# Kernel tuning notes

Hardware: AMD Instinct MI355X
Metric: run time of the kernel (lower is better)

Reference implementation:

```python
import jax, jax.numpy as jnp
import numpy as np

DIM = 1024
HEADS = 16
HEAD_DIM = DIM // HEADS


def rotate_half(x):
    x1, x2 = jnp.split(x, 2, axis=-1)
    return jnp.concatenate((-x2, x1), axis=-1)


def rope_tables(T, D, dtype=jnp.float32):
    inv_freq = 1.0 / (10000.0 ** (jnp.arange(0, D, 2, dtype=jnp.float32) / D))
    t = jnp.arange(T, dtype=jnp.float32)
    freqs = jnp.einsum('i,j->ij', t, inv_freq)  # [T, D/2]
    emb = jnp.concatenate((freqs, freqs), axis=-1)  # [T, D]
    return emb.astype(dtype), jnp.cos(emb).astype(dtype), jnp.sin(emb).astype(dtype)


def setup_inputs() -> dict:
    key = jax.random.key(0)
    kx, kq, kk, kv, ko = jax.random.split(key, 5)
    B, T = 2, 4096
    scale = 1.0 / np.sqrt(DIM)
    x = jax.random.normal(kx, (B, T, DIM), dtype=jnp.float32)
    wq = jax.random.normal(kq, (DIM, DIM), dtype=jnp.float32) * scale
    wk = jax.random.normal(kk, (DIM, DIM), dtype=jnp.float32) * scale
    wv = jax.random.normal(kv, (DIM, DIM), dtype=jnp.float32) * scale
    wo = jax.random.normal(ko, (DIM, DIM), dtype=jnp.float32) * scale
    return {"x": x, "wq": wq, "wk": wk, "wv": wv, "wo": wo}


def reference(x, wq, wk, wv, wo):
    B, T, C = x.shape
    H, D = HEADS, HEAD_DIM
    # projections; nn.Linear applies x @ W^T
    q = (x @ wq.T).reshape(B, T, H, D).transpose(0, 2, 1, 3)  # [B,H,T,D]
    k = (x @ wk.T).reshape(B, T, H, D).transpose(0, 2, 1, 3)
    v = (x @ wv.T).reshape(B, T, H, D).transpose(0, 2, 1, 3)
    _, cos, sin = rope_tables(T, D, x.dtype)
    cos = cos[None, None]  # [1,1,T,D]
    sin = sin[None, None]
    q = q * cos + rotate_half(q) * sin
    k = k * cos + rotate_half(k) * sin
    scores = jnp.einsum('bhtd,bhsd->bhts', q, k) / jnp.sqrt(jnp.asarray(D, x.dtype))
    attn = jax.nn.softmax(scores, axis=-1)
    out = jnp.einsum('bhts,bhsd->bhtd', attn, v)
    out = out.transpose(0, 2, 1, 3).reshape(B, T, C)
    return out @ wo.T
```

## Files before the change

kernel.cpp:

```cpp
#include <hip/hip_runtime.h>
#include <hip/hip_bf16.h>
#include <math.h>


typedef __attribute__((ext_vector_type(8))) short short8;
typedef __attribute__((ext_vector_type(4))) short short4v;
typedef __attribute__((ext_vector_type(4))) float floatx4;

using bf16 = __hip_bfloat16;

static constexpr int T_ = 4096;
static constexpr int C_ = 1024;
static constexpr int M_ = 8192;
static constexpr float QSCALE = 0.125f * 1.44269504088896340736f;

#if __has_builtin(__builtin_amdgcn_mfma_f32_16x16x16bf16_1k)
#define USE_K16 1
#else
#define USE_K16 0
#endif

#if __has_builtin(__builtin_amdgcn_exp2f)
#define EXP2 __builtin_amdgcn_exp2f
#else
#define EXP2 exp2f
#endif

__device__ __forceinline__ floatx4 mfma16(short8 a, short8 b, floatx4 c) {
    return __builtin_amdgcn_mfma_f32_16x16x32_bf16(a, b, c, 0, 0, 0);
}
#if USE_K16
__device__ __forceinline__ floatx4 mfma_k16(short4v a, short4v b, floatx4 c) {
    return __builtin_amdgcn_mfma_f32_16x16x16bf16_1k(a, b, c, 0, 0, 0);
}
#endif

__device__ __forceinline__ short8 ld8(const bf16* p) {
    return *reinterpret_cast<const short8*>(p);
}
__device__ __forceinline__ short4v ld4(const bf16* p) {
    return *reinterpret_cast<const short4v*>(p);
}
__device__ __forceinline__ void st8(bf16* p, short8 v) {
    *reinterpret_cast<short8*>(p) = v;
}
__device__ __forceinline__ unsigned short f2bf(float x) {
    bf16 h = __float2bfloat16(x);
    return reinterpret_cast<unsigned short&>(h);
}

__device__ __forceinline__ int pack2bf(float a, float b, unsigned sel) {
    const unsigned ua = __float_as_uint(a) + 0x8000u;
    const unsigned ub = __float_as_uint(b) + 0x8000u;
    int r;
    asm("v_perm_b32 %0, %1, %2, %3" : "=v"(r) : "v"(ub), "v"(ua), "s"(sel));
    return r;
}
__device__ __forceinline__ short4v i2s4(int lo, int hi) {
    union { int2 i; short4v s; } u;
    u.i.x = lo; u.i.y = hi;
    return u.s;
}
__device__ __forceinline__ short8 i2s8(int a, int b, int c, int d) {
    union { int4 i; short8 s; } u;
    u.i.x = a; u.i.y = b; u.i.z = c; u.i.w = d;
    return u.s;
}

__device__ __forceinline__ void cp16(const bf16* g, bf16* l) {
    __builtin_amdgcn_global_load_lds(
        (const __attribute__((address_space(1))) void*)g,
        (__attribute__((address_space(3))) void*)l, 16, 0, 0);
}

__global__ __launch_bounds__(256)
void prep_kernel(const float* __restrict__ x,
                 const float* __restrict__ wq, const float* __restrict__ wk,
                 const float* __restrict__ wv, const float* __restrict__ wo,
                 bf16* __restrict__ xb, bf16* __restrict__ wqb,
                 float2* __restrict__ CS) {
    const int blk = blockIdx.x;
    if (blk < 6144) {
        const float* in;
        bf16* out;
        int i;
        if (blk < 4096) {
            i = blk * 256 + threadIdx.x;
            in = x; out = xb;
        } else {
            i = (blk - 4096) * 256 + threadIdx.x;
            const int seg = i >> 17;
            const int off = i & 131071;
            in = (seg == 0) ? wq : (seg == 1) ? wk : (seg == 2) ? wv : wo;
            out = wqb + (size_t)i * 8 - (size_t)off * 8;
            i = off;
        }
        const float4* p = reinterpret_cast<const float4*>(in) + (size_t)i * 2;
        const float4 a = p[0];
        const float4 b = p[1];
        short8 v;
        v[0] = (short)f2bf(a.x); v[1] = (short)f2bf(a.y);
        v[2] = (short)f2bf(a.z); v[3] = (short)f2bf(a.w);
        v[4] = (short)f2bf(b.x); v[5] = (short)f2bf(b.y);
        v[6] = (short)f2bf(b.z); v[7] = (short)f2bf(b.w);
        *(reinterpret_cast<short8*>(out) + i) = v;
    } else {
        const int i = (blk - 6144) * 256 + threadIdx.x;
        const int t = i >> 5;
        const int j = i & 31;
        const float inv_freq = expf(-(float)j * 0.28782313662425575f);
        float s, c;
        sincosf((float)t * inv_freq, &s, &c);
        CS[i] = make_float2(c, s);
    }
}

__global__ __launch_bounds__(256)
void gemm128_kernel(const bf16* __restrict__ A, const bf16* __restrict__ W,
                    void* __restrict__ out, int mode, int ntile, int cpx) {
    const int orig = blockIdx.x;
    const int swz  = (orig & 7) * cpx + (orig >> 3);
    const int m0   = (swz / ntile) * 128;
    const int n0   = (swz % ntile) * 128;
    const int tid  = threadIdx.x;
    const int lane = tid & 63;
    const int wave = tid >> 6;
    const int quad = lane >> 4;
    const int lr   = lane & 15;
    const int wr   = (wave >> 1) * 64;
    const int wc   = (wave & 1) * 64;

    __shared__ __align__(16) bf16 Als[2][128 * 32];
    __shared__ __align__(16) bf16 Bls[2][128 * 32];

    const int srow = tid >> 2;
    const int scol = (tid & 3) * 8;

    floatx4 acc[4][4];
#pragma unroll
    for (int i = 0; i < 4; ++i)
#pragma unroll
        for (int j = 0; j < 4; ++j) acc[i][j] = floatx4{0.f, 0.f, 0.f, 0.f};

    const bf16* Ab = A + (size_t)m0 * C_;
    const bf16* Wb = W + (size_t)n0 * C_;

#pragma unroll
    for (int j = 0; j < 2; ++j) {
        const int row = srow + j * 64;
        cp16(Ab + (size_t)row * C_ + scol, &Als[0][(j * 256 + tid) * 8]);
        cp16(Wb + (size_t)row * C_ + scol, &Bls[0][(j * 256 + tid) * 8]);
    }
    __syncthreads();

    for (int k = 0; k < C_; k += 32) {
        const int buf = (k >> 5) & 1;
        if (k + 32 < C_) {
            const int nb = buf ^ 1;
#pragma unroll
            for (int j = 0; j < 2; ++j) {
                const int row = srow + j * 64;
                cp16(Ab + (size_t)row * C_ + k + 32 + scol,
                     &Als[nb][(j * 256 + tid) * 8]);
                cp16(Wb + (size_t)row * C_ + k + 32 + scol,
                     &Bls[nb][(j * 256 + tid) * 8]);
            }
        }

        short8 a[4], b[4];
#pragma unroll
        for (int i = 0; i < 4; ++i)
            a[i] = ld8(&Als[buf][(wr + i * 16 + lr) * 32 + quad * 8]);
#pragma unroll
        for (int j = 0; j < 4; ++j)
            b[j] = ld8(&Bls[buf][(wc + j * 16 + lr) * 32 + quad * 8]);
#pragma unroll
        for (int i = 0; i < 4; ++i)
#pragma unroll
            for (int j = 0; j < 4; ++j) acc[i][j] = mfma16(a[i], b[j], acc[i][j]);

        __syncthreads();
    }

    if (mode == 0) {
        bf16* ob = (bf16*)out;
#pragma unroll
        for (int j = 0; j < 4; ++j) {
            const int col = n0 + wc + j * 16 + lr;
#pragma unroll
            for (int i = 0; i < 4; ++i)
#pragma unroll
                for (int r = 0; r < 4; ++r) {
                    const int m = m0 + wr + i * 16 + quad * 4 + r;
                    ob[(size_t)m * C_ + col] = __float2bfloat16(acc[i][j][r]);
                }
        }
    } else {
        float* of = (float*)out;
#pragma unroll
        for (int j = 0; j < 4; ++j) {
            const int col = n0 + wc + j * 16 + lr;
#pragma unroll
            for (int i = 0; i < 4; ++i)
#pragma unroll
                for (int r = 0; r < 4; ++r) {
                    const int m = m0 + wr + i * 16 + quad * 4 + r;
                    of[(size_t)m * C_ + col] = acc[i][j][r];
                }
        }
    }
}

__global__ __launch_bounds__(256)
void gemm_qkv_kernel(const bf16* __restrict__ A, const bf16* __restrict__ W,
                     bf16* __restrict__ Qbase, const float2* __restrict__ CS) {
    const int orig = blockIdx.x;
    const int swz  = (orig & 7) * 192 + (orig >> 3);
    const int m0   = (swz / 24) * 128;
    const int n0g  = (swz % 24) * 128;
    const int tid  = threadIdx.x;
    const int lane = tid & 63;
    const int wave = tid >> 6;
    const int quad = lane >> 4;
    const int lr   = lane & 15;
    const int wr   = (wave >> 1) * 64;
    const int wc   = (wave & 1) * 64;

    __shared__ __align__(16) bf16 Als[2][128 * 32];
    __shared__ __align__(16) bf16 Bls[2][128 * 32];

    const int srow = tid >> 2;
    const int scol = (tid & 3) * 8;

    floatx4 acc[4][4];
#pragma unroll
    for (int i = 0; i < 4; ++i)
#pragma unroll
        for (int j = 0; j < 4; ++j) acc[i][j] = floatx4{0.f, 0.f, 0.f, 0.f};

    const bf16* Ab = A + (size_t)m0 * C_;
    const bf16* Wb = W + (size_t)n0g * C_;

#pragma unroll
    for (int j = 0; j < 2; ++j) {
        const int row = srow + j * 64;
        cp16(Ab + (size_t)row * C_ + scol, &Als[0][(j * 256 + tid) * 8]);
        cp16(Wb + (size_t)row * C_ + scol, &Bls[0][(j * 256 + tid) * 8]);
    }
    __syncthreads();

    for (int k = 0; k < C_; k += 32) {
        const int buf = (k >> 5) & 1;
        if (k + 32 < C_) {
            const int nb = buf ^ 1;
#pragma unroll
            for (int j = 0; j < 2; ++j) {
                const int row = srow + j * 64;
                cp16(Ab + (size_t)row * C_ + k + 32 + scol,
                     &Als[nb][(j * 256 + tid) * 8]);
                cp16(Wb + (size_t)row * C_ + k + 32 + scol,
                     &Bls[nb][(j * 256 + tid) * 8]);
            }
        }

        short8 a[4], b[4];
#pragma unroll
        for (int i = 0; i < 4; ++i)
            a[i] = ld8(&Als[buf][(wr + i * 16 + lr) * 32 + quad * 8]);
#pragma unroll
        for (int j = 0; j < 4; ++j)
            b[j] = ld8(&Bls[buf][(wc + j * 16 + lr) * 32 + quad * 8]);
#pragma unroll
        for (int i = 0; i < 4; ++i)
#pragma unroll
            for (int j = 0; j < 4; ++j) acc[i][j] = mfma16(a[i], b[j], acc[i][j]);

        __syncthreads();
    }

    const int seg = n0g >> 10;
    const int n0  = n0g & 1023;
    if (seg < 2) {
        bf16* ob = Qbase + (size_t)seg * M_ * C_;
        const float scale = (seg == 0) ? QSCALE : 1.0f;
        const int tb = (m0 & 4095) + wr + quad * 4;
#pragma unroll
        for (int j = 0; j < 2; ++j) {
            const int col  = n0 + wc + j * 16 + lr;
            const int jcol = j * 16 + lr;
#pragma unroll
            for (int i = 0; i < 4; ++i) {
#pragma unroll
                for (int r = 0; r < 4; ++r) {
                    const int t = tb + i * 16 + r;
                    const float2 cs = CS[t * 32 + jcol];
                    const float q1 = acc[i][j][r];
                    const float q2 = acc[i][j + 2][r];
                    const int m = m0 + wr + i * 16 + quad * 4 + r;
                    ob[(size_t)m * C_ + col] =
                        __float2bfloat16((q1 * cs.x - q2 * cs.y) * scale);
                    ob[(size_t)m * C_ + col + 32] =
                        __float2bfloat16((q2 * cs.x + q1 * cs.y) * scale);
                }
            }
        }
    } else {
        unsigned short* ob = (unsigned short*)(Qbase + (size_t)2 * M_ * C_);
        const int b2 = m0 >> 12;
#pragma unroll
        for (int j = 0; j < 4; ++j) {
            const int n = n0 + wc + j * 16 + lr;
            const int h = n >> 6;
            const int d = n & 63;
#pragma unroll
            for (int i = 0; i < 4; ++i) {
                const int t0 = (m0 & 4095) + wr + i * 16 + quad * 4;
                ushort4 v;
                v.x = f2bf(acc[i][j][0]); v.y = f2bf(acc[i][j][1]);
                v.z = f2bf(acc[i][j][2]); v.w = f2bf(acc[i][j][3]);
                size_t idx = ((size_t)((b2 * 16 + h) * 64 + d)) * T_ + t0;
                *reinterpret_cast<ushort4*>(ob + idx) = v;
            }
        }
    }
}

__global__ __launch_bounds__(256)
void attn_kernel(const bf16* __restrict__ Q, const bf16* __restrict__ K,
                 const bf16* __restrict__ Vt, bf16* __restrict__ AO) {
    const int tid  = threadIdx.x;
    const int lane = tid & 63;
    const int wave = tid >> 6;
    const int quad = lane >> 4;
    const int lr   = lane & 15;
    const int bh   = blockIdx.y;
    const int b    = bh >> 4;
    const int h    = bh & 15;
    const int q0   = blockIdx.x * 128 + wave * 32;

    const bf16* Qb = Q + (size_t)b * T_ * C_ + h * 64;
    const bf16* Kb = K + (size_t)b * T_ * C_ + h * 64;
    const bf16* Vb = Vt + (size_t)bh * 64 * T_;

#if USE_K16
    __shared__ __align__(16) bf16 Kls[2][64 * 64];
    __shared__ __align__(16) bf16 Vls[2][64 * 64];

    const int srow  = tid >> 3;
    const int sc    = tid & 7;
    const int sphys = (sc ^ (srow & 7)) * 8;
    const int soff0 = srow * 64 + sphys;
    const int soff1 = (srow + 32) * 64 + sphys;

    const unsigned psel = 0x07060302u;
    const floatx4 FZ = {0.f, 0.f, 0.f, 0.f};
    const int one2 = 0x3F803F80;
    const short8 VONE = i2s8(one2, one2, one2, one2);

    short8 aq[2][2];
#pragma unroll
    for (int t = 0; t < 2; ++t) {
        aq[t][0] = ld8(Qb + (size_t)(q0 + t * 16 + lr) * C_ + quad * 8);
        aq[t][1] = ld8(Qb + (size_t)(q0 + t * 16 + lr) * C_ + 32 + quad * 8);
    }

    floatx4 O[2][4];
#pragma unroll
    for (int t = 0; t < 2; ++t)
#pragma unroll
        for (int dt = 0; dt < 4; ++dt) O[t][dt] = floatx4{0.f, 0.f, 0.f, 0.f};
    floatx4 Osum[2] = {{0.f, 0.f, 0.f, 0.f}, {0.f, 0.f, 0.f, 0.f}};

    const int lr7    = lr & 7;
    const int kchunk = (quad ^ lr7) * 8;
    const int vsub   = (quad & 1) * 4;
    const int vbq    = quad >> 1;
    const int kel0   = lr * 64 + kchunk;
    const int kel1   = kel0 ^ 32;
    int velk[4];
#pragma unroll
    for (int kk = 0; kk < 4; ++kk)
        velk[kk] = lr * 64 + (((2 * kk + vbq) ^ lr7) * 8) + vsub;

    short8 kr0, kr1, vr0, vr1;
#define LOAD_STAGE(kv0)                                              \
    do {                                                             \
        kr0 = ld8(Kb + (size_t)((kv0) + srow) * C_ + sc * 8);        \
        kr1 = ld8(Kb + (size_t)((kv0) + srow + 32) * C_ + sc * 8);   \
        vr0 = ld8(Vb + (size_t)srow * T_ + (kv0) + sc * 8);          \
        vr1 = ld8(Vb + (size_t)(srow + 32) * T_ + (kv0) + sc * 8);   \
    } while (0)
#define STORE_STAGE(p)                                               \
    do {                                                             \
        st8(&Kls[p][soff0], kr0);                                    \
        st8(&Kls[p][soff1], kr1);                                    \
        st8(&Vls[p][soff0], vr0);                                    \
        st8(&Vls[p][soff1], vr1);                                    \
    } while (0)

#define BAR()                                                        \
    do {                                                             \
        asm volatile("s_waitcnt lgkmcnt(0)" ::: "memory");           \
        __builtin_amdgcn_s_barrier();                                \
    } while (0)

#define COMPUTE(P)                                                            \
    do {                                                                      \
        const bf16* Ks = Kls[P];                                              \
        const bf16* Vs = Vls[P];                                              \
        int prlo[2][4], prhi[2][4];                                           \
        _Pragma("unroll")                                                     \
        for (int kk = 0; kk < 4; ++kk) {                                      \
            const short8 kf0 = ld8(Ks + kk * 1024 + kel0);                    \
            const short8 kf1 = ld8(Ks + kk * 1024 + kel1);                    \
            floatx4 s0 = mfma16(kf0, aq[0][0], FZ);                           \
            s0 = mfma16(kf1, aq[0][1], s0);                                   \
            floatx4 s1 = mfma16(kf0, aq[1][0], FZ);                           \
            s1 = mfma16(kf1, aq[1][1], s1);                                   \
            const float e0 = EXP2(s0[0]), e1 = EXP2(s0[1]);                   \
            const float e2 = EXP2(s0[2]), e3 = EXP2(s0[3]);                   \
            prlo[0][kk] = pack2bf(e0, e1, psel);                              \
            prhi[0][kk] = pack2bf(e2, e3, psel);                              \
            const float f0 = EXP2(s1[0]), f1 = EXP2(s1[1]);                   \
            const float f2 = EXP2(s1[2]), f3 = EXP2(s1[3]);                   \
            prlo[1][kk] = pack2bf(f0, f1, psel);                              \
            prhi[1][kk] = pack2bf(f2, f3, psel);                              \
        }                                                                     \
        \
        Osum[0] = mfma16(i2s8(prlo[0][0], prhi[0][0], prlo[0][1], prhi[0][1]),\
                         VONE, Osum[0]);                                      \
        Osum[0] = mfma16(i2s8(prlo[0][2], prhi[0][2], prlo[0][3], prhi[0][3]),\
                         VONE, Osum[0]);                                      \
        Osum[1] = mfma16(i2s8(prlo[1][0], prhi[1][0], prlo[1][1], prhi[1][1]),\
                         VONE, Osum[1]);                                      \
        Osum[1] = mfma16(i2s8(prlo[1][2], prhi[1][2], prlo[1][3], prhi[1][3]),\
                         VONE, Osum[1]);                                      \
        __builtin_amdgcn_s_setprio(1);                                        \
        _Pragma("unroll")                                                     \
        for (int dt = 0; dt < 4; ++dt) {                                      \
            _Pragma("unroll")                                                 \
            for (int kk = 0; kk < 4; ++kk) {                                  \
                const short4v vf = ld4(Vs + dt * 1024 + velk[kk]);            \
                O[0][dt] = mfma_k16(i2s4(prlo[0][kk], prhi[0][kk]), vf, O[0][dt]); \
                O[1][dt] = mfma_k16(i2s4(prlo[1][kk], prhi[1][kk]), vf, O[1][dt]); \
            }                                                                 \
        }                                                                     \
        __builtin_amdgcn_s_setprio(0);                                        \
    } while (0)

    LOAD_STAGE(0);
    STORE_STAGE(0);
    LOAD_STAGE(64);
    BAR();

    constexpr int NS = T_ / 64;
    for (int s = 0; s < NS; s += 2) {
        if (s + 1 < NS) STORE_STAGE(1);
        if (s + 2 < NS) LOAD_STAGE((s + 2) * 64);
        COMPUTE(0);
        BAR();
        if (s + 2 < NS) STORE_STAGE(0);
        if (s + 3 < NS) LOAD_STAGE((s + 3) * 64);
        COMPUTE(1);
        BAR();
    }

#pragma unroll
    for (int t = 0; t < 2; ++t) {
#pragma unroll
        for (int r = 0; r < 4; ++r) {
            const float inv = 1.0f / fmaxf(Osum[t][r], 1e-30f);
            const size_t row =
                (size_t)(b * T_ + q0 + t * 16 + quad * 4 + r) * C_ + h * 64;
            AO[row + 0  + lr] = __float2bfloat16(O[t][0][r] * inv);
            AO[row + 16 + lr] = __float2bfloat16(O[t][1][r] * inv);
            AO[row + 32 + lr] = __float2bfloat16(O[t][2][r] * inv);
            AO[row + 48 + lr] = __float2bfloat16(O[t][3][r] * inv);
        }
    }
#undef LOAD_STAGE
#undef STORE_STAGE
#undef COMPUTE
#undef BAR
#else
    __shared__ __align__(16) unsigned short Pbuf[4][512];
    unsigned short* Pw = Pbuf[wave];
    for (int half = 0; half < 2; ++half) {
        const int qh = q0 + half * 16;
        const short8 aq0 = ld8(Qb + (size_t)(qh + lr) * C_ + quad * 8);
        const short8 aq1 = ld8(Qb + (size_t)(qh + lr) * C_ + 32 + quad * 8);
        floatx4 O0 = {0,0,0,0}, O1 = {0,0,0,0}, O2 = {0,0,0,0}, O3 = {0,0,0,0};
        float lrun[4] = {0.f, 0.f, 0.f, 0.f};
        for (int kv = 0; kv < T_; kv += 32) {
            floatx4 S0 = {0,0,0,0}, S1 = {0,0,0,0};
            const bf16* k0 = Kb + (size_t)(kv + lr) * C_ + quad * 8;
            const bf16* k1 = Kb + (size_t)(kv + 16 + lr) * C_ + quad * 8;
            S0 = mfma16(aq0, ld8(k0), S0);
            S0 = mfma16(aq1, ld8(k0 + 32), S0);
            S1 = mfma16(aq0, ld8(k1), S1);
            S1 = mfma16(aq1, ld8(k1 + 32), S1);
#pragma unroll
            for (int r = 0; r < 4; ++r) {
                const float e0 = exp2f(S0[r]);
                const float e1 = exp2f(S1[r]);
                lrun[r] += e0 + e1;
                const int row = quad * 4 + r;
                Pw[row * 32 + lr]      = f2bf(e0);
                Pw[row * 32 + 16 + lr] = f2bf(e1);
            }
            __syncthreads();
            const short8 ap = *reinterpret_cast<const short8*>(Pw + lr * 32 + quad * 8);
            O0 = mfma16(ap, ld8(Vb + (size_t)(lr)      * T_ + kv + quad * 8), O0);
            O1 = mfma16(ap, ld8(Vb + (size_t)(16 + lr) * T_ + kv + quad * 8), O1);
            O2 = mfma16(ap, ld8(Vb + (size_t)(32 + lr) * T_ + kv + quad * 8), O2);
            O3 = mfma16(ap, ld8(Vb + (size_t)(48 + lr) * T_ + kv + quad * 8), O3);
            __syncthreads();
        }
#pragma unroll
        for (int r = 0; r < 4; ++r) {
            float l = lrun[r];
            l += __shfl_xor(l, 1); l += __shfl_xor(l, 2);
            l += __shfl_xor(l, 4); l += __shfl_xor(l, 8);
            const float inv = 1.0f / fmaxf(l, 1e-30f);
            const size_t row = (size_t)(b * T_ + qh + quad * 4 + r) * C_ + h * 64;
            AO[row + 0  + lr] = __float2bfloat16(O0[r] * inv);
            AO[row + 16 + lr] = __float2bfloat16(O1[r] * inv);
            AO[row + 32 + lr] = __float2bfloat16(O2[r] * inv);
            AO[row + 48 + lr] = __float2bfloat16(O3[r] * inv);
        }
    }
#endif
}

extern "C" void kernel_launch(void* const* d_in, const int* in_sizes, int n_in,
                              void* d_out, int out_size, void* d_ws, size_t ws_size,
                              hipStream_t stream) {
    const float* x  = (const float*)d_in[0];
    const float* wq = (const float*)d_in[1];
    const float* wk = (const float*)d_in[2];
    const float* wv = (const float*)d_in[3];
    const float* wo = (const float*)d_in[4];
    float* out = (float*)d_out;

    bf16* xb  = (bf16*)d_ws;
    bf16* wqb = xb  + (size_t)M_ * C_;
    bf16* wkb = wqb + (size_t)C_ * C_;
    bf16* wvb = wkb + (size_t)C_ * C_;
    bf16* wob = wvb + (size_t)C_ * C_;
    bf16* Q   = wob + (size_t)C_ * C_;
    bf16* K   = Q   + (size_t)M_ * C_;
    bf16* Vt  = K   + (size_t)M_ * C_;
    float2* CS = (float2*)(Vt + (size_t)M_ * C_);
    bf16* AO  = xb;

    prep_kernel<<<6656, 256, 0, stream>>>(x, wq, wk, wv, wo, xb, wqb, CS);

    gemm_qkv_kernel<<<1536, 256, 0, stream>>>(xb, wqb, Q, CS);

    attn_kernel<<<dim3(T_ / 128, 32), 256, 0, stream>>>(Q, K, Vt, AO);

    gemm128_kernel<<<512, 256, 0, stream>>>(AO, wob, out, 2, 8, 64);
}
```

Before: 392.8 us.

## Triple-buffer GEMM shared-memory tiles with one barrier per k-step and explicit vmcnt waits

Both projection GEMM kernels move from a double-buffered LDS pipeline with two syncthreads per step to a three-stage ring buffer. Loads run two k-steps ahead, each step waits with an explicit s_waitcnt vmcnt followed by a single s_barrier, and the main loop is unrolled by three. The aim is to hide global-to-LDS latency and cut barrier stalls. The cost is extra LDS per block (48KB instead of 32KB), which could lower occupancy. Correctness depends on the hand-chosen vmcnt values matching the number of async copies in flight.

```diff
diff --git a/kernel.cpp b/kernel.cpp
--- a/kernel.cpp
+++ b/kernel.cpp
@@ -115,6 +115,60 @@
     }
 }
 
+#define GEMM_PROLOGUE(Ab, Wb)                                                 \
+    _Pragma("unroll")                                                         \
+    for (int j = 0; j < 2; ++j) {                                             \
+        const int row = srow + j * 64;                                        \
+        cp16((Ab) + (size_t)row * C_ + scol, &Als[0][(j * 256 + tid) * 8]);   \
+        cp16((Wb) + (size_t)row * C_ + scol, &Bls[0][(j * 256 + tid) * 8]);   \
+    }                                                                         \
+    _Pragma("unroll")                                                         \
+    for (int j = 0; j < 2; ++j) {                                             \
+        const int row = srow + j * 64;                                        \
+        cp16((Ab) + (size_t)row * C_ + 32 + scol, &Als[1][(j * 256 + tid) * 8]); \
+        cp16((Wb) + (size_t)row * C_ + 32 + scol, &Bls[1][(j * 256 + tid) * 8]); \
+    }
+
+#define KSTEP(Ab, Wb, KK, BUF, LB, DOISSUE, VMN)                              \
+    do {                                                                      \
+        asm volatile("s_waitcnt vmcnt(" VMN ")" ::: "memory");                \
+        __builtin_amdgcn_sched_barrier(0);                                    \
+        __builtin_amdgcn_s_barrier();                                         \
+        __builtin_amdgcn_sched_barrier(0);                                    \
+        if (DOISSUE) {                                                        \
+            _Pragma("unroll")                                                 \
+            for (int j = 0; j < 2; ++j) {                                     \
+                const int row = srow + j * 64;                                \
+                cp16((Ab) + (size_t)row * C_ + (KK) + 64 + scol,              \
+                     &Als[LB][(j * 256 + tid) * 8]);                          \
+                cp16((Wb) + (size_t)row * C_ + (KK) + 64 + scol,              \
+                     &Bls[LB][(j * 256 + tid) * 8]);                          \
+            }                                                                 \
+        }                                                                     \
+        short8 a[4], b[4];                                                    \
+        _Pragma("unroll")                                                     \
+        for (int i = 0; i < 4; ++i)                                           \
+            a[i] = ld8(&Als[BUF][(wr + i * 16 + lr) * 32 + quad * 8]);        \
+        _Pragma("unroll")                                                     \
+        for (int j = 0; j < 4; ++j)                                           \
+            b[j] = ld8(&Bls[BUF][(wc + j * 16 + lr) * 32 + quad * 8]);        \
+        _Pragma("unroll")                                                     \
+        for (int i = 0; i < 4; ++i)                                           \
+            _Pragma("unroll")                                                 \
+            for (int j = 0; j < 4; ++j)                                       \
+                acc[i][j] = mfma16(a[i], b[j], acc[i][j]);                    \
+    } while (0)
+
+#define GEMM_MAINLOOP(Ab, Wb)                                                 \
+    GEMM_PROLOGUE(Ab, Wb)                                                     \
+    for (int kk = 0; kk < 960; kk += 96) {                                    \
+        KSTEP(Ab, Wb, kk,      0, 2, 1, "4");                                 \
+        KSTEP(Ab, Wb, kk + 32, 1, 0, 1, "4");                                 \
+        KSTEP(Ab, Wb, kk + 64, 2, 1, 1, "4");                                 \
+    }                                                                         \
+    KSTEP(Ab, Wb, 960, 0, 2, 0, "4");                                         \
+    KSTEP(Ab, Wb, 992, 1, 0, 0, "0");
+
 __global__ __launch_bounds__(256)
 void gemm128_kernel(const bf16* __restrict__ A, const bf16* __restrict__ W,
                     void* __restrict__ out, int mode, int ntile, int cpx) {
@@ -130,8 +184,8 @@
     const int wr   = (wave >> 1) * 64;
     const int wc   = (wave & 1) * 64;
 
-    __shared__ __align__(16) bf16 Als[2][128 * 32];
-    __shared__ __align__(16) bf16 Bls[2][128 * 32];
+    __shared__ __align__(16) bf16 Als[3][128 * 32];
+    __shared__ __align__(16) bf16 Bls[3][128 * 32];
 
     const int srow = tid >> 2;
     const int scol = (tid & 3) * 8;
@@ -145,42 +199,7 @@
     const bf16* Ab = A + (size_t)m0 * C_;
     const bf16* Wb = W + (size_t)n0 * C_;
 
-#pragma unroll
-    for (int j = 0; j < 2; ++j) {
-        const int row = srow + j * 64;
-        cp16(Ab + (size_t)row * C_ + scol, &Als[0][(j * 256 + tid) * 8]);
-        cp16(Wb + (size_t)row * C_ + scol, &Bls[0][(j * 256 + tid) * 8]);
-    }
-    __syncthreads();
-
-    for (int k = 0; k < C_; k += 32) {
-        const int buf = (k >> 5) & 1;
-        if (k + 32 < C_) {
-            const int nb = buf ^ 1;
-#pragma unroll
-            for (int j = 0; j < 2; ++j) {
-                const int row = srow + j * 64;
-                cp16(Ab + (size_t)row * C_ + k + 32 + scol,
-                     &Als[nb][(j * 256 + tid) * 8]);
-                cp16(Wb + (size_t)row * C_ + k + 32 + scol,
-                     &Bls[nb][(j * 256 + tid) * 8]);
-            }
-        }
-
-        short8 a[4], b[4];
-#pragma unroll
-        for (int i = 0; i < 4; ++i)
-            a[i] = ld8(&Als[buf][(wr + i * 16 + lr) * 32 + quad * 8]);
-#pragma unroll
-        for (int j = 0; j < 4; ++j)
-            b[j] = ld8(&Bls[buf][(wc + j * 16 + lr) * 32 + quad * 8]);
-#pragma unroll
-        for (int i = 0; i < 4; ++i)
-#pragma unroll
-            for (int j = 0; j < 4; ++j) acc[i][j] = mfma16(a[i], b[j], acc[i][j]);
-
-        __syncthreads();
-    }
+    GEMM_MAINLOOP(Ab, Wb)
 
     if (mode == 0) {
         bf16* ob = (bf16*)out;
@@ -226,8 +245,8 @@
     const int wr   = (wave >> 1) * 64;
     const int wc   = (wave & 1) * 64;
 
-    __shared__ __align__(16) bf16 Als[2][128 * 32];
-    __shared__ __align__(16) bf16 Bls[2][128 * 32];
+    __shared__ __align__(16) bf16 Als[3][128 * 32];
+    __shared__ __align__(16) bf16 Bls[3][128 * 32];
 
     const int srow = tid >> 2;
     const int scol = (tid & 3) * 8;
@@ -241,42 +260,7 @@
     const bf16* Ab = A + (size_t)m0 * C_;
     const bf16* Wb = W + (size_t)n0g * C_;
 
-#pragma unroll
-    for (int j = 0; j < 2; ++j) {
-        const int row = srow + j * 64;
-        cp16(Ab + (size_t)row * C_ + scol, &Als[0][(j * 256 + tid) * 8]);
-        cp16(Wb + (size_t)row * C_ + scol, &Bls[0][(j * 256 + tid) * 8]);
-    }
-    __syncthreads();
-
-    for (int k = 0; k < C_; k += 32) {
-        const int buf = (k >> 5) & 1;
-        if (k + 32 < C_) {
-            const int nb = buf ^ 1;
-#pragma unroll
-            for (int j = 0; j < 2; ++j) {
-                const int row = srow + j * 64;
-                cp16(Ab + (size_t)row * C_ + k + 32 + scol,
-                     &Als[nb][(j * 256 + tid) * 8]);
-                cp16(Wb + (size_t)row * C_ + k + 32 + scol,
-                     &Bls[nb][(j * 256 + tid) * 8]);
-            }
-        }
-
-        short8 a[4], b[4];
-#pragma unroll
-        for (int i = 0; i < 4; ++i)
-            a[i] = ld8(&Als[buf][(wr + i * 16 + lr) * 32 + quad * 8]);
-#pragma unroll
-        for (int j = 0; j < 4; ++j)
-            b[j] = ld8(&Bls[buf][(wc + j * 16 + lr) * 32 + quad * 8]);
-#pragma unroll
-        for (int i = 0; i < 4; ++i)
-#pragma unroll
-            for (int j = 0; j < 4; ++j) acc[i][j] = mfma16(a[i], b[j], acc[i][j]);
-
-        __syncthreads();
-    }
+    GEMM_MAINLOOP(Ab, Wb)
 
     const int seg = n0g >> 10;
     const int n0  = n0g & 1023;
```

Measured after the change: 376.1 us. -4.2%, faster.
